# Optimization experiments

Hardware: AMD Instinct MI355X
Metric: run time of the kernel (lower is better)

Reference implementation:

```python
import jax, jax.numpy as jnp
import numpy as np
from jax import lax

FACTOR = 2
BLUR_K = [1.0, 3.0, 3.0, 1.0]

def _make_kernel(k, factor):
    k = jnp.asarray(k, dtype=jnp.float32)
    k = k[None, :] * k[:, None]          # outer product -> [4,4]
    k = k / jnp.sum(k)
    return k * (factor ** 2)

def setup_inputs() -> dict:
    key = jax.random.key(0)
    x = jax.random.normal(key, (32, 512, 512, 1), dtype=jnp.float32)  # NHWC, C must be 1
    kernel = _make_kernel(BLUR_K, FACTOR)                              # [4,4]
    return {"x": x, "kernel": kernel}

def reference(x, kernel):
    # nearest-neighbor upsample by FACTOR (matches tf.image.resize nearest for integer factor)
    up = jnp.repeat(jnpp if False else jnp.repeat(x, FACTOR, axis=1), FACTOR, axis=2)
    w = kernel.reshape(1, -1, 1, 1)  # [fh=1, fw=16, in=1, out=1] (HWIO)
    out = lax.conv_general_dilated(
        up, w,
        window_strides=(1, 1),
        padding='SAME',
        dimension_numbers=('NHWC', 'HWIO', 'NHWC'),
    )
    return out
```

## Files before the change

### kernel.cpp

```cpp
#include <hip/hip_runtime.h>


#define W_IN   512
#define H_IN   512
#define NB     32
#define W_OUT  1024
#define NPAIR  (NB * H_IN / 2)
#define NBLK   2048
#define ITERS  (NPAIR / NBLK)

typedef float f32x4 __attribute__((ext_vector_type(4)));

__global__ __launch_bounds__(256) void upsample_blur_kernel(
    const float* __restrict__ x,
    const float* __restrict__ kern,
    float* __restrict__ out)
{
    __shared__ float rows[2][2][520];

    const int t = threadIdx.x;

    if (t < 32) {
        const int b  = t >> 4;
        const int rr = (t >> 3) & 1;
        const int i  = t & 7;
        rows[b][rr][(i < 4) ? i : (512 + i)] = 0.0f;
    }

    float kf[16];
#pragma unroll
    for (int i = 0; i < 16; ++i) kf[i] = kern[i];

    float we[9], wo[8];
    we[0] = kf[0];
#pragma unroll
    for (int i = 0; i < 7; ++i) we[i + 1] = kf[2 * i + 1] + kf[2 * i + 2];
    we[8] = kf[15];
#pragma unroll
    for (int i = 0; i < 8; ++i) wo[i] = kf[2 * i] + kf[2 * i + 1];

    const int rsel = t >> 7;
    const int csel = (4 * t) & 511;

    int buf = 0;
#pragma unroll
    for (int it = 0; it < ITERS; ++it) {
        const int pairIdx = blockIdx.x + it * NBLK;

        const f32x4 xi = __builtin_nontemporal_load(
            reinterpret_cast<const f32x4*>(x + (size_t)pairIdx * (2 * W_IN)) + t);
        *reinterpret_cast<f32x4*>(&rows[buf][rsel][4 + csel]) = xi;

        __syncthreads();

        float v0[10], v1[10];
#pragma unroll
        for (int i = 0; i < 10; ++i) v0[i] = rows[buf][0][2 * t + i];
#pragma unroll
        for (int i = 0; i < 10; ++i) v1[i] = rows[buf][1][2 * t + i];

        float a0 = 0.f, a1 = 0.f, a2 = 0.f, a3 = 0.f;
        float b0 = 0.f, b1 = 0.f, b2 = 0.f, b3 = 0.f;
#pragma unroll
        for (int j = 0; j < 9; ++j) { a0 += we[j] * v0[j];     b0 += we[j] * v1[j];     }
#pragma unroll
        for (int j = 0; j < 8; ++j) { a1 += wo[j] * v0[j + 1]; b1 += wo[j] * v1[j + 1]; }
#pragma unroll
        for (int j = 0; j < 9; ++j) { a2 += we[j] * v0[j + 1]; b2 += we[j] * v1[j + 1]; }
#pragma unroll
        for (int j = 0; j < 8; ++j) { a3 += wo[j] * v0[j + 2]; b3 += wo[j] * v1[j + 2]; }

        f32x4 oa; oa.x = a0; oa.y = a1; oa.z = a2; oa.w = a3;
        f32x4 ob; ob.x = b0; ob.y = b1; ob.z = b2; ob.w = b3;

        f32x4* o4 = reinterpret_cast<f32x4*>(out + (size_t)pairIdx * (4 * W_OUT));
        __builtin_nontemporal_store(oa, o4 + t);
        __builtin_nontemporal_store(oa, o4 + 256 + t);
        __builtin_nontemporal_store(ob, o4 + 512 + t);
        __builtin_nontemporal_store(ob, o4 + 768 + t);

        buf ^= 1;
    }
}

extern "C" void kernel_launch(void* const* d_in, const int* in_sizes, int n_in,
                              void* d_out, int out_size, void* d_ws, size_t ws_size,
                              hipStream_t stream) {
    const float* x    = (const float*)d_in[0];
    const float* kern = (const float*)d_in[1];
    float* out        = (float*)d_out;

    upsample_blur_kernel<<<NBLK, 256, 0, stream>>>(x, kern, out);
}
```

Measured before the change: 157.9 us.

## Replace LDS staging with direct overlapping global loads, one row pair per block

Removes the shared-memory staging buffer and __syncthreads. Each thread now loads three overlapping float4 chunks of its input row straight from global memory, zero-filling the edges, and computes 8 outputs in registers. The grid grows to one block per row pair instead of a persistent loop over several pairs. Nontemporal loads and stores are replaced with plain ones. This adds redundant global loads (handled by the cache) and more block launches, and each thread now writes two adjacent float4s, which is less coalesced than before.

Result: no change. 158.2 us (+0.2%).

```diff
diff --git a/kernel.cpp b/kernel.cpp
--- a/kernel.cpp
+++ b/kernel.cpp
@@ -6,8 +6,6 @@
 #define NB     32
 #define W_OUT  1024
 #define NPAIR  (NB * H_IN / 2)
-#define NBLK   2048
-#define ITERS  (NPAIR / NBLK)
 
 typedef float f32x4 __attribute__((ext_vector_type(4)));
 
@@ -16,16 +14,23 @@
     const float* __restrict__ kern,
     float* __restrict__ out)
 {
-    __shared__ float rows[2][2][520];
+    const int t    = threadIdx.x;
+    const int rsel = t >> 7;
+    const int s    = t & 127;
 
-    const int t = threadIdx.x;
+    const int p      = blockIdx.x;
+    const int rowIn  = 2 * p + rsel;
 
-    if (t < 32) {
-        const int b  = t >> 4;
-        const int rr = (t >> 3) & 1;
-        const int i  = t & 7;
-        rows[b][rr][(i < 4) ? i : (512 + i)] = 0.0f;
-    }
+    const float* xr = x + (size_t)rowIn * W_IN;
+    const f32x4 zero = {0.f, 0.f, 0.f, 0.f};
+    const f32x4 cA = (s == 0)   ? zero : *reinterpret_cast<const f32x4*>(xr + 4 * s - 4);
+    const f32x4 cB =                     *reinterpret_cast<const f32x4*>(xr + 4 * s);
+    const f32x4 cC = (s == 127) ? zero : *reinterpret_cast<const f32x4*>(xr + 4 * s + 4);
+
+    float V[12];
+    V[0] = cA.x; V[1]  = cA.y; V[2]  = cA.z; V[3]  = cA.w;
+    V[4] = cB.x; V[5]  = cB.y; V[6]  = cB.z; V[7]  = cB.w;
+    V[8] = cC.x; V[9]  = cC.y; V[10] = cC.z; V[11] = cC.w;
 
     float kf[16];
 #pragma unroll
@@ -39,48 +44,28 @@
 #pragma unroll
     for (int i = 0; i < 8; ++i) wo[i] = kf[2 * i] + kf[2 * i + 1];
 
-    const int rsel = t >> 7;
-    const int csel = (4 * t) & 511;
+    float o[8];
+#pragma unroll
+    for (int c = 0; c < 8; c += 2) {
+        float accE = 0.f, accO = 0.f;
+        const int se = c / 2;
+        const int so = c / 2 + 1;
+#pragma unroll
+        for (int j = 0; j < 9; ++j) accE += we[j] * V[j + se];
+#pragma unroll
+        for (int j = 0; j < 8; ++j) accO += wo[j] * V[j + so];
+        o[c]     = accE;
+        o[c + 1] = accO;
+    }
 
-    int buf = 0;
-#pragma unroll
-    for (int it = 0; it < ITERS; ++it) {
-        const int pairIdx = blockIdx.x + it * NBLK;
+    f32x4 lo; lo.x = o[0]; lo.y = o[1]; lo.z = o[2]; lo.w = o[3];
+    f32x4 hi; hi.x = o[4]; hi.y = o[5]; hi.z = o[6]; hi.w = o[7];
 
-        const f32x4 xi = __builtin_nontemporal_load(
-            reinterpret_cast<const f32x4*>(x + (size_t)pairIdx * (2 * W_IN)) + t);
-        *reinterpret_cast<f32x4*>(&rows[buf][rsel][4 + csel]) = xi;
-
-        __syncthreads();
-
-        float v0[10], v1[10];
-#pragma unroll
-        for (int i = 0; i < 10; ++i) v0[i] = rows[buf][0][2 * t + i];
-#pragma unroll
-        for (int i = 0; i < 10; ++i) v1[i] = rows[buf][1][2 * t + i];
-
-        float a0 = 0.f, a1 = 0.f, a2 = 0.f, a3 = 0.f;
-        float b0 = 0.f, b1 = 0.f, b2 = 0.f, b3 = 0.f;
-#pragma unroll
-        for (int j = 0; j < 9; ++j) { a0 += we[j] * v0[j];     b0 += we[j] * v1[j];     }
-#pragma unroll
-        for (int j = 0; j < 8; ++j) { a1 += wo[j] * v0[j + 1]; b1 += wo[j] * v1[j + 1]; }
-#pragma unroll
-        for (int j = 0; j < 9; ++j) { a2 += we[j] * v0[j + 1]; b2 += we[j] * v1[j + 1]; }
-#pragma unroll
-        for (int j = 0; j < 8; ++j) { a3 += wo[j] * v0[j + 2]; b3 += wo[j] * v1[j + 2]; }
-
-        f32x4 oa; oa.x = a0; oa.y = a1; oa.z = a2; oa.w = a3;
-        f32x4 ob; ob.x = b0; ob.y = b1; ob.z = b2; ob.w = b3;
-
-        f32x4* o4 = reinterpret_cast<f32x4*>(out + (size_t)pairIdx * (4 * W_OUT));
-        __builtin_nontemporal_store(oa, o4 + t);
-        __builtin_nontemporal_store(oa, o4 + 256 + t);
-        __builtin_nontemporal_store(ob, o4 + 512 + t);
-        __builtin_nontemporal_store(ob, o4 + 768 + t);
-
-        buf ^= 1;
-    }
+    const size_t ob = ((size_t)(4 * p + 2 * rsel)) * W_OUT + 8 * s;
+    *reinterpret_cast<f32x4*>(out + ob)             = lo;
+    *reinterpret_cast<f32x4*>(out + ob + 4)         = hi;
+    *reinterpret_cast<f32x4*>(out + ob + W_OUT)     = lo;
+    *reinterpret_cast<f32x4*>(out + ob + W_OUT + 4) = hi;
 }
 
 extern "C" void kernel_launch(void* const* d_in, const int* in_sizes, int n_in,
@@ -90,5 +75,5 @@
     const float* kern = (const float*)d_in[1];
     float* out        = (float*)d_out;
 
-    upsample_blur_kernel<<<NBLK, 256, 0, stream>>>(x, kern, out);
+    upsample_blur_kernel<<<NPAIR, 256, 0, stream>>>(x, kern, out);
 }
```
